# Performance work log

Measured on AMD Instinct MI355X. Metric: run time of the kernel, lower is better.

## Reference

```python
import jax, jax.numpy as jnp
import numpy as np

N_PL = 16      # PiecewiseLin resolution
OBJECTS = 10   # top-k objects kept / max count


def plin(w, x):
    """PiecewiseLin forward: w is [N_PL+1], x is any-shape tensor in [0,1]."""
    w = jnp.abs(w)
    w = w / w.sum()
    csum = jnp.cumsum(w)                     # [N_PL+1]
    y = N_PL * x
    idx = y.astype(jnp.int32)                # trunc toward zero (x >= 0)
    f = y - jnp.trunc(y)                     # fractional part
    lo = csum[jnp.minimum(idx, N_PL)]
    hi = w[jnp.minimum(idx + 1, N_PL)]
    return lo + f * hi


def _area(box):  # box: [n, 4, o]
    return jnp.clip(box[:, 2] - box[:, 0], 0.0, None) * jnp.clip(box[:, 3] - box[:, 1], 0.0, None)


def _iou(a, b):  # a, b: [n, 4, o] -> [n, o, o]
    mn = jnp.maximum(a[:, :2, :, None], b[:, :2, None, :])
    mx = jnp.minimum(a[:, 2:, :, None], b[:, 2:, None, :])
    wh = jnp.clip(mx - mn, 0.0, None)
    inter = wh[:, 0] * wh[:, 1]
    aa = _area(a)[:, :, None]
    ab = _area(b)[:, None, :]
    return inter / (aa + ab - inter + 1e-12)


def counter_forward(boxes, attention, ws):
    n = boxes.shape[0]
    # filter_most_important: top-k by attention
    att, idx = jax.lax.top_k(attention, OBJECTS)                       # [n, o]
    idx_b = jnp.broadcast_to(idx[:, None, :], (n, 4, OBJECTS))
    boxes = jnp.take_along_axis(boxes, idx_b, axis=2)                  # [n, 4, o]
    att = jax.nn.sigmoid(att)                                          # already_sigmoided=False

    relev = att[:, :, None] * att[:, None, :]                          # [n, o, o]
    dist = 1.0 - _iou(boxes, boxes)                                    # [n, o, o]

    score = plin(ws[0], relev) * plin(ws[1], dist)
    dedup = plin(ws[3], relev) * plin(ws[4], dist)

    # deduplicate
    att_diff = jnp.abs(att[:, :, None] - att[:, None, :])              # [n, o, o]
    score_diff = jnp.abs(dedup[..., :, None] - dedup[..., None, :])    # [n, o, o, o]
    sim = plin(ws[2], 1.0 - score_diff).prod(axis=1) * plin(ws[2], 1.0 - att_diff)  # [n, o, o]
    row_sims = sim.sum(axis=2)                                         # [n, o]
    all_sims = row_sims[:, :, None] * row_sims[:, None, :]             # [n, o, o]

    score = score / all_sims
    correction = plin(ws[0], att * att) / row_sims                     # [n, o]
    total = score.sum(axis=(1, 2))[:, None] + correction.sum(axis=1, keepdims=True)  # [n, 1]
    total = jnp.sqrt(total + 1e-20)

    # to_one_hot
    s = jnp.clip(total, 0.0, float(OBJECTS))                           # [n, 1]
    i = s.astype(jnp.int32)[:, 0]
    f = s - jnp.trunc(s)
    tl = jax.nn.one_hot(jnp.minimum(i, OBJECTS), OBJECTS + 1, dtype=s.dtype)
    tr = jax.nn.one_hot(jnp.minimum(i + 1, OBJECTS), OBJECTS + 1, dtype=s.dtype)
    one_hot = (1.0 - f) * tl + f * tr                                  # [n, o+1]

    # confidence
    att_conf = jnp.abs(plin(ws[5], att) - 0.5)                         # [n, o]
    dist_conf = jnp.abs(plin(ws[6], dist) - 0.5)                       # [n, o, o]
    conf = plin(ws[7], att_conf.mean(axis=1, keepdims=True)
                + dist_conf.mean(axis=2).mean(axis=1, keepdims=True))  # [n, 1]
    return one_hot * conf                                              # [n, o+1]


def setup_inputs() -> dict:
    key = jax.random.key(0)
    k1, k2, k3 = jax.random.split(key, 3)
    n, m = 32768, 36
    boxes = jax.random.uniform(k1, (n, 4, m), dtype=jnp.float32)
    attention = jax.random.normal(k2, (n, m), dtype=jnp.float32)
    ws = jax.random.uniform(k3, (8, N_PL + 1), dtype=jnp.float32, minval=0.1, maxval=1.0)
    return {"boxes": boxes, "attention": attention, "ws": ws}


def reference(boxes, attention, ws):
    return counter_forward(boxes, attention, ws)
```

## Files before the change

kernel.cpp:

```cpp
#include <hip/hip_runtime.h>
#include <math.h>

#define N_PL 16
#define NT   17
#define OBJ  10
#define M    36
#define SPB  8
#define BLK  64

__constant__ unsigned char c_p55[55] = {
 0x00,0x01,0x02,0x03,0x04,0x05,0x06,0x07,0x08,0x09,
 0x11,0x12,0x13,0x14,0x15,0x16,0x17,0x18,0x19,
 0x22,0x23,0x24,0x25,0x26,0x27,0x28,0x29,
 0x33,0x34,0x35,0x36,0x37,0x38,0x39,
 0x44,0x45,0x46,0x47,0x48,0x49,
 0x55,0x56,0x57,0x58,0x59,
 0x66,0x67,0x68,0x69,
 0x77,0x78,0x79,
 0x88,0x89,
 0x99};
__constant__ unsigned char c_p45[45] = {
 0x01,0x02,0x03,0x04,0x05,0x06,0x07,0x08,0x09,
 0x12,0x13,0x14,0x15,0x16,0x17,0x18,0x19,
 0x23,0x24,0x25,0x26,0x27,0x28,0x29,
 0x34,0x35,0x36,0x37,0x38,0x39,
 0x45,0x46,0x47,0x48,0x49,
 0x56,0x57,0x58,0x59,
 0x67,0x68,0x69,
 0x78,0x79,
 0x89};

__device__ __forceinline__ float plin_tab(const float* s_tab, int t, float x) {
    const float* wn = s_tab + t * NT;
    const float* cs = s_tab + 136 + t * NT;
    float y = 16.0f * x;
    int idx = (int)y;
    float f = y - (float)idx;
    int i0 = idx < N_PL ? idx : N_PL;
    int i1 = (idx + 1) < N_PL ? (idx + 1) : N_PL;
    return __builtin_fmaf(f, wn[i1], cs[i0]);
}

__global__ void prep_tables(const float* __restrict__ ws, float* __restrict__ tab) {
    int t = threadIdx.x;
    if (t < 8) {
        float w[NT]; float sum = 0.f;
        #pragma unroll
        for (int k = 0; k < NT; ++k) { w[k] = fabsf(ws[t * NT + k]); sum += w[k]; }
        float c = 0.f;
        #pragma unroll
        for (int k = 0; k < NT; ++k) {
            float v = w[k] / sum;
            tab[t * NT + k] = v;
            c += v;
            tab[136 + t * NT + k] = c;
        }
    }
}

__global__ __launch_bounds__(BLK, 4) void counter_kernel(
    const float* __restrict__ boxes,
    const float* __restrict__ attn,
    const float* __restrict__ tab,
    float* __restrict__ out,
    int n)
{
    __shared__ float s_tab[272];
    __shared__ float s_att[OBJ][SPB];
    __shared__ float s_box[5][OBJ][SPB];
    __shared__ float s_dedup[OBJ * OBJ][SPB];
    __shared__ float s_rowp[OBJ][BLK];
    __shared__ float s_rfin[OBJ][SPB];

    const int tid = threadIdx.x;
    const int g = tid & 7;
    const int p = tid >> 3;

    #pragma unroll
    for (int k = 0; k < 5; ++k) {
        int idx = tid + k * BLK;
        if (idx < 272) s_tab[idx] = tab[idx];
    }
    #pragma unroll
    for (int i = 0; i < OBJ; ++i) s_rowp[i][tid] = 0.f;

    int s = blockIdx.x * SPB + p;
    const bool active = (s < n);
    if (!active) s = n - 1;

    const float* arow = attn + (size_t)s * M;
    float v[M];
    #pragma unroll
    for (int k = 0; k < 9; ++k) {
        float4 t4 = ((const float4*)arow)[k];
        v[4*k+0] = t4.x; v[4*k+1] = t4.y; v[4*k+2] = t4.z; v[4*k+3] = t4.w;
    }
    unsigned long long key[M];
    #pragma unroll
    for (int m = 0; m < M; ++m) {
        unsigned int b = __float_as_uint(v[m]);
        unsigned int u = b ^ (0x80000000u | (unsigned int)((int)b >> 31));
        key[m] = ((unsigned long long)u << 6) | (unsigned int)(63 - m);
    }
    unsigned long long myk[5] = {0ull,0ull,0ull,0ull,0ull};
    #pragma unroll
    for (int m = 0; m < M; ++m)
        if ((m & 7) == g) myk[m >> 3] = key[m];
    int rnk[5] = {0,0,0,0,0};
    #pragma unroll
    for (int m = 0; m < M; ++m) {
        #pragma unroll
        for (int k = 0; k < 5; ++k) rnk[k] += (key[m] > myk[k]) ? 1 : 0;
    }

    __syncthreads();

    float mA = 0.f;
    const float* brow = boxes + (size_t)s * (4 * M);
    #pragma unroll
    for (int k = 0; k < 5; ++k) {
        int e = g + 8 * k;
        if (e < M && rnk[k] < OBJ) {
            unsigned int u = (unsigned int)(myk[k] >> 6);
            unsigned int b = (u & 0x80000000u) ? (u ^ 0x80000000u) : ~u;
            float ve = __uint_as_float(b);
            float a = 1.f / (1.f + __expf(-ve));
            int r = rnk[k];
            s_att[r][p] = a;
            mA += fabsf(plin_tab(s_tab, 5, a) - 0.5f);
            float x0 = brow[e], y0 = brow[M + e], x1 = brow[2 * M + e], y1 = brow[3 * M + e];
            float bw = fmaxf(x1 - x0, 0.f), bh = fmaxf(y1 - y0, 0.f);
            s_box[0][r][p] = x0; s_box[1][r][p] = y0;
            s_box[2][r][p] = x1; s_box[3][r][p] = y1;
            s_box[4][r][p] = bw * bh;
        }
    }
    __syncthreads();

    float mD = 0.f;
    float sc_loc[7];
    #pragma unroll
    for (int t = 0; t < 7; ++t) {
        int q = g + 8 * t;
        bool act = (q < 55);
        int pk = c_p55[act ? q : 0];
        int i = pk >> 4, j = pk & 15;
        float x0i = s_box[0][i][p], y0i = s_box[1][i][p], x1i = s_box[2][i][p], y1i = s_box[3][i][p], ari = s_box[4][i][p];
        float x0j = s_box[0][j][p], y0j = s_box[1][j][p], x1j = s_box[2][j][p], y1j = s_box[3][j][p], arj = s_box[4][j][p];
        float wx = fminf(x1i, x1j) - fmaxf(x0i, x0j); wx = fmaxf(wx, 0.f);
        float wy = fminf(y1i, y1j) - fmaxf(y0i, y0j); wy = fmaxf(wy, 0.f);
        float inter = wx * wy;
        float un = ari + arj - inter + 1e-12f;
        float d = 1.f - inter * __builtin_amdgcn_rcpf(un);
        float ai = s_att[i][p], aj = s_att[j][p];
        float relev = ai * aj;
        float dd = plin_tab(s_tab, 3, relev) * plin_tab(s_tab, 4, d);
        sc_loc[t] = plin_tab(s_tab, 0, relev) * plin_tab(s_tab, 1, d);
        float dc = fabsf(plin_tab(s_tab, 6, d) - 0.5f);
        if (act) {
            s_dedup[i * OBJ + j][p] = dd;
            s_dedup[j * OBJ + i][p] = dd;
            mD += (i != j) ? 2.f * dc : dc;
        }
    }
    __syncthreads();

    #pragma unroll
    for (int t = 0; t < 6; ++t) {
        int r = g + 8 * t;
        bool act = (r < 45);
        int pk = c_p45[act ? r : 0];
        int i = pk >> 4, j = pk & 15;
        float ai = s_att[i][p], aj = s_att[j][p];
        float prod = plin_tab(s_tab, 2, 1.f - fabsf(ai - aj));
        #pragma unroll
        for (int a = 0; a < OBJ; ++a) {
            float da = fabsf(s_dedup[a * OBJ + i][p] - s_dedup[a * OBJ + j][p]);
            prod *= plin_tab(s_tab, 2, 1.f - da);
        }
        if (act) {
            s_rowp[i][tid] += prod;
            s_rowp[j][tid] += prod;
        }
    }
    __syncthreads();

    {
        float c16 = s_tab[136 + 2 * NT + N_PL];
        float c2 = c16 * c16, c4 = c2 * c2, c8 = c4 * c4;
        float diag = c8 * c2 * c16;
        int base = tid & ~7;
        #pragma unroll
        for (int rep = 0; rep < 2; ++rep) {
            int i = g + 8 * rep;
            if (i < OBJ) {
                float sum = diag;
                #pragma unroll
                for (int l = 0; l < 8; ++l) sum += s_rowp[i][base + l];
                s_rfin[i][p] = 1.f / sum;
            }
        }
    }
    __syncthreads();

    float tot = 0.f;
    #pragma unroll
    for (int t = 0; t < 7; ++t) {
        int q = g + 8 * t;
        bool act = (q < 55);
        int pk = c_p55[act ? q : 0];
        int i = pk >> 4, j = pk & 15;
        float term = sc_loc[t] * s_rfin[i][p] * s_rfin[j][p];
        if (act) tot += (i != j) ? 2.f * term : term;
    }
    #pragma unroll
    for (int rep = 0; rep < 2; ++rep) {
        int i = g + 8 * rep;
        if (i < OBJ) {
            float ai = s_att[i][p];
            tot += plin_tab(s_tab, 0, ai * ai) * s_rfin[i][p];
        }
    }
    float carg = mA * 0.1f + mD * 0.01f;
    tot  += __shfl_xor(tot, 1);  tot  += __shfl_xor(tot, 2);  tot  += __shfl_xor(tot, 4);
    carg += __shfl_xor(carg, 1); carg += __shfl_xor(carg, 2); carg += __shfl_xor(carg, 4);

    float total = sqrtf(tot + 1e-20f);
    float conf = plin_tab(s_tab, 7, carg);
    float scl = fminf(fmaxf(total, 0.f), 10.f);
    int i0 = (int)scl;
    float f = scl - (float)i0;
    int lo = i0 < OBJ ? i0 : OBJ;
    int hi = (i0 + 1) < OBJ ? (i0 + 1) : OBJ;

    if (active) {
        float* orow = out + (size_t)s * (OBJ + 1);
        {
            int c = g;
            float vv = ((c == lo) ? (1.f - f) : 0.f) + ((c == hi) ? f : 0.f);
            orow[c] = vv * conf;
        }
        if (g < 3) {
            int c = g + 8;
            float vv = ((c == lo) ? (1.f - f) : 0.f) + ((c == hi) ? f : 0.f);
            orow[c] = vv * conf;
        }
    }
}

extern "C" void kernel_launch(void* const* d_in, const int* in_sizes, int n_in,
                              void* d_out, int out_size, void* d_ws, size_t ws_size,
                              hipStream_t stream) {
    const float* boxes = (const float*)d_in[0];
    const float* attn  = (const float*)d_in[1];
    const float* ws    = (const float*)d_in[2];
    float* out = (float*)d_out;
    float* tab = (float*)d_ws;
    int n = in_sizes[1] / M;
    hipLaunchKernelGGL(prep_tables, dim3(1), dim3(64), 0, stream, ws, tab);
    int blocks = (n + SPB - 1) / SPB;
    hipLaunchKernelGGL(counter_kernel, dim3(blocks), dim3(BLK), 0, stream,
                       boxes, attn, tab, out, n);
}
```

Measured before the change: 87.85 us.

## Use 16 threads per sample, fuse table prep, and register-shuffle row sums

Each sample now gets 16 threads instead of 8, so a 64-thread block covers 4 samples and the per-thread pair work shrinks. The separate prep_tables launch is removed and every block builds the normalized weight and cumsum tables in shared memory itself. Top-k ranking streams float4 loads and compares them on the fly instead of holding 36 keys in registers. Row sums are kept in register arrays and reduced with warp shuffles instead of a shared-memory array plus a barrier. The cost is more blocks, redundant table building in every block, and 10-way shuffle reductions per thread.

```diff
diff --git a/kernel.cpp b/kernel.cpp
--- a/kernel.cpp
+++ b/kernel.cpp
@@ -5,7 +5,7 @@
 #define NT   17
 #define OBJ  10
 #define M    36
-#define SPB  8
+#define SPB  4
 #define BLK  64
 
 __constant__ unsigned char c_p55[55] = {
@@ -41,27 +41,16 @@
     return __builtin_fmaf(f, wn[i1], cs[i0]);
 }
 
-__global__ void prep_tables(const float* __restrict__ ws, float* __restrict__ tab) {
-    int t = threadIdx.x;
-    if (t < 8) {
-        float w[NT]; float sum = 0.f;
-        #pragma unroll
-        for (int k = 0; k < NT; ++k) { w[k] = fabsf(ws[t * NT + k]); sum += w[k]; }
-        float c = 0.f;
-        #pragma unroll
-        for (int k = 0; k < NT; ++k) {
-            float v = w[k] / sum;
-            tab[t * NT + k] = v;
-            c += v;
-            tab[136 + t * NT + k] = c;
-        }
-    }
-}
-
-__global__ __launch_bounds__(BLK, 4) void counter_kernel(
+__device__ __forceinline__ unsigned long long mkkey(float v, int m) {
+    unsigned int b = __float_as_uint(v);
+    unsigned int u = b ^ (0x80000000u | (unsigned int)((int)b >> 31));
+    return ((unsigned long long)u << 6) | (unsigned int)(63 - m);
+}
+
+__global__ __launch_bounds__(BLK, 6) void counter_kernel(
     const float* __restrict__ boxes,
     const float* __restrict__ attn,
-    const float* __restrict__ tab,
+    const float* __restrict__ ws,
     float* __restrict__ out,
     int n)
 {
@@ -69,91 +58,90 @@
     __shared__ float s_att[OBJ][SPB];
     __shared__ float s_box[5][OBJ][SPB];
     __shared__ float s_dedup[OBJ * OBJ][SPB];
-    __shared__ float s_rowp[OBJ][BLK];
     __shared__ float s_rfin[OBJ][SPB];
 
     const int tid = threadIdx.x;
-    const int g = tid & 7;
-    const int p = tid >> 3;
-
-    #pragma unroll
-    for (int k = 0; k < 5; ++k) {
-        int idx = tid + k * BLK;
-        if (idx < 272) s_tab[idx] = tab[idx];
-    }
-    #pragma unroll
-    for (int i = 0; i < OBJ; ++i) s_rowp[i][tid] = 0.f;
+    const int g = tid & 15;
+    const int p = tid >> 4;
+
+    if (tid < 8) {
+        float w[NT]; float sum = 0.f;
+        #pragma unroll
+        for (int k = 0; k < NT; ++k) { w[k] = fabsf(ws[tid * NT + k]); sum += w[k]; }
+        float rs = 1.f / sum;
+        float c = 0.f;
+        #pragma unroll
+        for (int k = 0; k < NT; ++k) {
+            float v = w[k] * rs;
+            s_tab[tid * NT + k] = v;
+            c += v;
+            s_tab[136 + tid * NT + k] = c;
+        }
+    }
 
     int s = blockIdx.x * SPB + p;
     const bool active = (s < n);
     if (!active) s = n - 1;
 
     const float* arow = attn + (size_t)s * M;
-    float v[M];
-    #pragma unroll
-    for (int k = 0; k < 9; ++k) {
-        float4 t4 = ((const float4*)arow)[k];
-        v[4*k+0] = t4.x; v[4*k+1] = t4.y; v[4*k+2] = t4.z; v[4*k+3] = t4.w;
-    }
-    unsigned long long key[M];
-    #pragma unroll
-    for (int m = 0; m < M; ++m) {
-        unsigned int b = __float_as_uint(v[m]);
-        unsigned int u = b ^ (0x80000000u | (unsigned int)((int)b >> 31));
-        key[m] = ((unsigned long long)u << 6) | (unsigned int)(63 - m);
-    }
-    unsigned long long myk[5] = {0ull,0ull,0ull,0ull,0ull};
-    #pragma unroll
-    for (int m = 0; m < M; ++m)
-        if ((m & 7) == g) myk[m >> 3] = key[m];
-    int rnk[5] = {0,0,0,0,0};
-    #pragma unroll
-    for (int m = 0; m < M; ++m) {
-        #pragma unroll
-        for (int k = 0; k < 5; ++k) rnk[k] += (key[m] > myk[k]) ? 1 : 0;
-    }
-
-    __syncthreads();
-
+    float mv[3]; unsigned long long myk[3];
+    #pragma unroll
+    for (int k = 0; k < 3; ++k) {
+        int e = g + 16 * k;
+        bool ok = e < M;
+        float v = ok ? arow[e] : 0.f;
+        mv[k] = v;
+        myk[k] = ok ? mkkey(v, e) : 0ull;
+    }
+    int rnk0 = 0, rnk1 = 0, rnk2 = 0;
+    #pragma unroll
+    for (int c4 = 0; c4 < 9; ++c4) {
+        float4 t4 = ((const float4*)arow)[c4];
+        float vv[4] = {t4.x, t4.y, t4.z, t4.w};
+        #pragma unroll
+        for (int q = 0; q < 4; ++q) {
+            unsigned long long kk = mkkey(vv[q], 4 * c4 + q);
+            rnk0 += (kk > myk[0]) ? 1 : 0;
+            rnk1 += (kk > myk[1]) ? 1 : 0;
+            rnk2 += (kk > myk[2]) ? 1 : 0;
+        }
+    }
+    int rnk[3] = {rnk0, rnk1, rnk2};
+
+    __syncthreads();
+
+    const float* brow = boxes + (size_t)s * (4 * M);
     float mA = 0.f;
-    const float* brow = boxes + (size_t)s * (4 * M);
-    #pragma unroll
-    for (int k = 0; k < 5; ++k) {
-        int e = g + 8 * k;
+    #pragma unroll
+    for (int k = 0; k < 3; ++k) {
+        int e = g + 16 * k;
         if (e < M && rnk[k] < OBJ) {
-            unsigned int u = (unsigned int)(myk[k] >> 6);
-            unsigned int b = (u & 0x80000000u) ? (u ^ 0x80000000u) : ~u;
-            float ve = __uint_as_float(b);
-            float a = 1.f / (1.f + __expf(-ve));
+            float a = 1.f / (1.f + __expf(-mv[k]));
             int r = rnk[k];
             s_att[r][p] = a;
             mA += fabsf(plin_tab(s_tab, 5, a) - 0.5f);
             float x0 = brow[e], y0 = brow[M + e], x1 = brow[2 * M + e], y1 = brow[3 * M + e];
-            float bw = fmaxf(x1 - x0, 0.f), bh = fmaxf(y1 - y0, 0.f);
             s_box[0][r][p] = x0; s_box[1][r][p] = y0;
             s_box[2][r][p] = x1; s_box[3][r][p] = y1;
-            s_box[4][r][p] = bw * bh;
+            s_box[4][r][p] = fmaxf(x1 - x0, 0.f) * fmaxf(y1 - y0, 0.f);
         }
     }
     __syncthreads();
 
     float mD = 0.f;
-    float sc_loc[7];
-    #pragma unroll
-    for (int t = 0; t < 7; ++t) {
-        int q = g + 8 * t;
+    float sc_loc[4];
+    #pragma unroll
+    for (int t = 0; t < 4; ++t) {
+        int q = g + 16 * t;
         bool act = (q < 55);
         int pk = c_p55[act ? q : 0];
         int i = pk >> 4, j = pk & 15;
-        float x0i = s_box[0][i][p], y0i = s_box[1][i][p], x1i = s_box[2][i][p], y1i = s_box[3][i][p], ari = s_box[4][i][p];
-        float x0j = s_box[0][j][p], y0j = s_box[1][j][p], x1j = s_box[2][j][p], y1j = s_box[3][j][p], arj = s_box[4][j][p];
-        float wx = fminf(x1i, x1j) - fmaxf(x0i, x0j); wx = fmaxf(wx, 0.f);
-        float wy = fminf(y1i, y1j) - fmaxf(y0i, y0j); wy = fmaxf(wy, 0.f);
-        float inter = wx * wy;
-        float un = ari + arj - inter + 1e-12f;
+        float wx = fminf(s_box[2][i][p], s_box[2][j][p]) - fmaxf(s_box[0][i][p], s_box[0][j][p]);
+        float wy = fminf(s_box[3][i][p], s_box[3][j][p]) - fmaxf(s_box[1][i][p], s_box[1][j][p]);
+        float inter = fmaxf(wx, 0.f) * fmaxf(wy, 0.f);
+        float un = s_box[4][i][p] + s_box[4][j][p] - inter + 1e-12f;
         float d = 1.f - inter * __builtin_amdgcn_rcpf(un);
-        float ai = s_att[i][p], aj = s_att[j][p];
-        float relev = ai * aj;
+        float relev = s_att[i][p] * s_att[j][p];
         float dd = plin_tab(s_tab, 3, relev) * plin_tab(s_tab, 4, d);
         sc_loc[t] = plin_tab(s_tab, 0, relev) * plin_tab(s_tab, 1, d);
         float dc = fabsf(plin_tab(s_tab, 6, d) - 0.5f);
@@ -165,65 +153,63 @@
     }
     __syncthreads();
 
-    #pragma unroll
-    for (int t = 0; t < 6; ++t) {
-        int r = g + 8 * t;
-        bool act = (r < 45);
-        int pk = c_p45[act ? r : 0];
+    float racc[OBJ];
+    #pragma unroll
+    for (int r = 0; r < OBJ; ++r) racc[r] = 0.f;
+    #pragma unroll
+    for (int t = 0; t < 3; ++t) {
+        int q = g + 16 * t;
+        bool act = (q < 45);
+        int pk = c_p45[act ? q : 0];
         int i = pk >> 4, j = pk & 15;
-        float ai = s_att[i][p], aj = s_att[j][p];
-        float prod = plin_tab(s_tab, 2, 1.f - fabsf(ai - aj));
+        float prod = plin_tab(s_tab, 2, 1.f - fabsf(s_att[i][p] - s_att[j][p]));
         #pragma unroll
         for (int a = 0; a < OBJ; ++a) {
             float da = fabsf(s_dedup[a * OBJ + i][p] - s_dedup[a * OBJ + j][p]);
             prod *= plin_tab(s_tab, 2, 1.f - da);
         }
-        if (act) {
-            s_rowp[i][tid] += prod;
-            s_rowp[j][tid] += prod;
-        }
-    }
-    __syncthreads();
-
+        if (!act) prod = 0.f;
+        #pragma unroll
+        for (int r = 0; r < OBJ; ++r)
+            racc[r] += ((r == i) || (r == j)) ? prod : 0.f;
+    }
+    #pragma unroll
+    for (int r = 0; r < OBJ; ++r) {
+        float v = racc[r];
+        v += __shfl_xor(v, 1); v += __shfl_xor(v, 2);
+        v += __shfl_xor(v, 4); v += __shfl_xor(v, 8);
+        racc[r] = v;
+    }
     {
         float c16 = s_tab[136 + 2 * NT + N_PL];
         float c2 = c16 * c16, c4 = c2 * c2, c8 = c4 * c4;
         float diag = c8 * c2 * c16;
-        int base = tid & ~7;
-        #pragma unroll
-        for (int rep = 0; rep < 2; ++rep) {
-            int i = g + 8 * rep;
-            if (i < OBJ) {
-                float sum = diag;
-                #pragma unroll
-                for (int l = 0; l < 8; ++l) sum += s_rowp[i][base + l];
-                s_rfin[i][p] = 1.f / sum;
-            }
-        }
+        float myrow = racc[0];
+        #pragma unroll
+        for (int r = 1; r < OBJ; ++r) myrow = (g == r) ? racc[r] : myrow;
+        if (g < OBJ) s_rfin[g][p] = 1.f / (myrow + diag);
     }
     __syncthreads();
 
     float tot = 0.f;
     #pragma unroll
-    for (int t = 0; t < 7; ++t) {
-        int q = g + 8 * t;
+    for (int t = 0; t < 4; ++t) {
+        int q = g + 16 * t;
         bool act = (q < 55);
         int pk = c_p55[act ? q : 0];
         int i = pk >> 4, j = pk & 15;
         float term = sc_loc[t] * s_rfin[i][p] * s_rfin[j][p];
         if (act) tot += (i != j) ? 2.f * term : term;
     }
-    #pragma unroll
-    for (int rep = 0; rep < 2; ++rep) {
-        int i = g + 8 * rep;
-        if (i < OBJ) {
-            float ai = s_att[i][p];
-            tot += plin_tab(s_tab, 0, ai * ai) * s_rfin[i][p];
-        }
+    if (g < OBJ) {
+        float ai = s_att[g][p];
+        tot += plin_tab(s_tab, 0, ai * ai) * s_rfin[g][p];
     }
     float carg = mA * 0.1f + mD * 0.01f;
-    tot  += __shfl_xor(tot, 1);  tot  += __shfl_xor(tot, 2);  tot  += __shfl_xor(tot, 4);
-    carg += __shfl_xor(carg, 1); carg += __shfl_xor(carg, 2); carg += __shfl_xor(carg, 4);
+    tot  += __shfl_xor(tot, 1);  tot  += __shfl_xor(tot, 2);
+    tot  += __shfl_xor(tot, 4);  tot  += __shfl_xor(tot, 8);
+    carg += __shfl_xor(carg, 1); carg += __shfl_xor(carg, 2);
+    carg += __shfl_xor(carg, 4); carg += __shfl_xor(carg, 8);
 
     float total = sqrtf(tot + 1e-20f);
     float conf = plin_tab(s_tab, 7, carg);
@@ -233,18 +219,9 @@
     int lo = i0 < OBJ ? i0 : OBJ;
     int hi = (i0 + 1) < OBJ ? (i0 + 1) : OBJ;
 
-    if (active) {
-        float* orow = out + (size_t)s * (OBJ + 1);
-        {
-            int c = g;
-            float vv = ((c == lo) ? (1.f - f) : 0.f) + ((c == hi) ? f : 0.f);
-            orow[c] = vv * conf;
-        }
-        if (g < 3) {
-            int c = g + 8;
-            float vv = ((c == lo) ? (1.f - f) : 0.f) + ((c == hi) ? f : 0.f);
-            orow[c] = vv * conf;
-        }
+    if (active && g <= OBJ) {
+        float vv = ((g == lo) ? (1.f - f) : 0.f) + ((g == hi) ? f : 0.f);
+        out[(size_t)s * (OBJ + 1) + g] = vv * conf;
     }
 }
 
@@ -255,10 +232,8 @@
     const float* attn  = (const float*)d_in[1];
     const float* ws    = (const float*)d_in[2];
     float* out = (float*)d_out;
-    float* tab = (float*)d_ws;
     int n = in_sizes[1] / M;
-    hipLaunchKernelGGL(prep_tables, dim3(1), dim3(64), 0, stream, ws, tab);
     int blocks = (n + SPB - 1) / SPB;
     hipLaunchKernelGGL(counter_kernel, dim3(blocks), dim3(BLK), 0, stream,
-                       boxes, attn, tab, out, n);
-}
+                       boxes, attn, ws, out, n);
+}
```

New measurement: 122.9 us. 1.4x slower.
